# Performance work log

Hardware: AMD Instinct MI355X
Metric: run time of the kernel (lower is better)

## Reference

```python
import jax, jax.numpy as jnp
import numpy as np
import math

B, L, D, H = 2, 2048, 1024, 16
DH = D // H  # d_head = 64
FACTOR = 5


def setup_inputs() -> dict:
    key = jax.random.key(0)
    ks = jax.random.split(key, 6)
    s = 0.02
    x = jax.random.normal(ks[0], (B, L, D), jnp.float32)
    Wq = jax.random.normal(ks[1], (D, D), jnp.float32) * s
    bq = jnp.zeros((D,), jnp.float32)
    Wkv = jax.random.normal(ks[2], (2 * D, D), jnp.float32) * s
    bkv = jnp.zeros((2 * D,), jnp.float32)
    Wout = jax.random.normal(ks[3], (D, D), jnp.float32) * s
    bout = jnp.zeros((D,), jnp.float32)
    U = min(FACTOR * math.ceil(math.log(L)), L)  # 40
    index_sample = jax.random.randint(ks[4], (L, U), 0, L, dtype=jnp.int32)
    return {"x": x, "Wq": Wq, "bq": bq, "Wkv": Wkv, "bkv": bkv,
            "Wout": Wout, "bout": bout, "index_sample": index_sample,
            "factor": FACTOR}


def reference(x, Wq, bq, Wkv, bkv, Wout, bout, index_sample, factor):
    b, l, d = x.shape
    h, dh = H, DH
    scale = 1.0 / math.sqrt(dh)
    u = min(factor * math.ceil(math.log(l)), l)

    # projections (torch Linear: y = x @ W.T + b)
    Q = (x @ Wq.T + bq).reshape(b, l, h, dh).transpose(0, 2, 1, 3)   # [B,H,L,dh]
    KV = x @ Wkv.T + bkv
    K, V = jnp.split(KV, 2, axis=-1)
    K = K.reshape(b, l, h, dh).transpose(0, 2, 1, 3)                  # [B,H,L,dh]
    V = V.reshape(b, l, h, dh).transpose(0, 2, 1, 3)                  # [B,H,L,dh]

    # sampled QK: per query position l, dot with U sampled keys
    K_s = K[:, :, index_sample, :]                                    # [B,H,L,U,dh]
    QK = jnp.einsum('bhld,bhlud->bhlu', Q, K_s)                       # [B,H,L,U]
    M = QK.max(axis=-1) - QK.mean(axis=-1)                            # sparsity measure
    _, top_idx = jax.lax.top_k(M, u)                                  # [B,H,u]

    # full attention only for the top-u queries
    top_q = jnp.take_along_axis(Q, top_idx[..., None], axis=2)        # [B,H,u,dh]
    scores = jnp.einsum('bhud,bhkd->bhuk', top_q, K) * scale          # [B,H,u,L]
    attn = jax.nn.softmax(scores, axis=-1)
    ctx_update = jnp.einsum('bhuk,bhkd->bhud', attn, V)               # [B,H,u,dh]

    # mean-initialized context, scatter updates at top queries
    context = jnp.broadcast_to(V.mean(axis=2, keepdims=True), (b, h, l, dh))
    bI = jnp.arange(b)[:, None, None]
    hI = jnp.arange(h)[None, :, None]
    context = context.at[bI, hI, top_idx].set(ctx_update)             # [B,H,L,dh]

    context = context.transpose(0, 2, 1, 3).reshape(b, l, d)
    return context @ Wout.T + bout
```

## Files before the change

kernel.cpp:

```cpp
#include <hip/hip_runtime.h>
#include <math.h>

#define B_ 2
#define L_ 2048
#define D_ 1024
#define H_ 16
#define DH_ 64
#define U_ 40
#define SCALE_ 0.125f

typedef __attribute__((ext_vector_type(8))) short short8v;
typedef __attribute__((ext_vector_type(4))) float f32x4;
typedef __attribute__((ext_vector_type(4))) unsigned short ushort4v;

static __device__ __forceinline__ unsigned short bf16_rne(float f) {
  unsigned int u = __float_as_uint(f);
  u += 0x7fff + ((u >> 16) & 1);
  return (unsigned short)(u >> 16);
}
static __device__ __forceinline__ float bf16_f32(unsigned short h) {
  return __uint_as_float(((unsigned int)h) << 16);
}

static __device__ __forceinline__ void gload16(const unsigned short* src,
                                               unsigned short* lds) {
  __builtin_amdgcn_global_load_lds(
      (const __attribute__((address_space(1))) void*)src,
      (__attribute__((address_space(3))) void*)lds, 16, 0, 0);
}

#define FENCE asm volatile("" ::: "memory")
#define BARRIER                        \
  do {                                 \
    FENCE;                             \
    __builtin_amdgcn_s_barrier();      \
    FENCE;                             \
  } while (0)
#define LGKM0                                             \
  do {                                                    \
    asm volatile("s_waitcnt lgkmcnt(0)" ::: "memory");    \
    __builtin_amdgcn_sched_barrier(0);                    \
  } while (0)

__global__ __launch_bounds__(256) void split_all(
    const float* __restrict__ Wq, const float* __restrict__ Wkv,
    const float* __restrict__ X, unsigned short* __restrict__ Whi,
    unsigned short* __restrict__ Wlo, unsigned short* __restrict__ Xhi,
    unsigned short* __restrict__ Xlo, float* __restrict__ vmAcc, int nW) {
  if (blockIdx.x == 0) {
    for (int z = threadIdx.x; z < B_ * D_; z += 256) vmAcc[z] = 0.f;
  }
  int i = blockIdx.x * 256 + threadIdx.x;
  const int nq_q = (D_ * D_) / 4;
  float4 v;
  unsigned short *hi, *lo;
  int off;
  if (i < nW) {
    v = (i < nq_q) ? ((const float4*)Wq)[i] : ((const float4*)Wkv)[i - nq_q];
    hi = Whi; lo = Wlo; off = i;
  } else {
    off = i - nW;
    v = ((const float4*)X)[off];
    hi = Xhi; lo = Xlo;
  }
  float vv[4] = {v.x, v.y, v.z, v.w};
  ushort4v h, l;
#pragma unroll
  for (int e = 0; e < 4; ++e) {
    unsigned short hh = bf16_rne(vv[e]);
    h[e] = hh;
    l[e] = bf16_rne(vv[e] - bf16_f32(hh));
  }
  ((ushort4v*)hi)[off] = h;
  ((ushort4v*)lo)[off] = l;
}

__global__ __launch_bounds__(512, 2) void gemm_qkv_8ph(
    const unsigned short* __restrict__ Xhi,
    const unsigned short* __restrict__ Xlo,
    const unsigned short* __restrict__ Whi,
    const unsigned short* __restrict__ Wlo,
    const float* __restrict__ bq, const float* __restrict__ bkv,
    float* __restrict__ Qo, float* __restrict__ Ko, float* __restrict__ Vo,
    float* __restrict__ vmAcc) {
  __shared__ unsigned short LDS[3][20480];
  const int tid = threadIdx.x;
  const int lane = tid & 63;
  const int wave = tid >> 6;
  const int wm = wave >> 2, wn = wave & 3;
  const int row0 = blockIdx.y * 128;
  const int col0 = blockIdx.x * 192;

  f32x4 acc[4][3] = {};

  const unsigned short* gsrc[5];
#pragma unroll
  for (int r = 0; r < 5; ++r) {
    int c = wave + 8 * r;
    const unsigned short* base;
    int rowin, isA;
    if (c < 8)       { base = Xhi; rowin = c * 16;        isA = 1; }
    else if (c < 16) { base = Xlo; rowin = (c - 8) * 16;  isA = 1; }
    else if (c < 28) { base = Whi; rowin = (c - 16) * 16; isA = 0; }
    else             { base = Wlo; rowin = (c - 28) * 16; isA = 0; }
    rowin += (lane >> 2);
    int grow = (isA ? row0 : col0) + rowin;
    int seg = (lane & 3) ^ ((rowin >> 1) & 3);
    gsrc[r] = base + (size_t)grow * D_ + seg * 8;
  }

  const int fr_r = lane & 15;
  const int hs = lane >> 4;

#define RD_A(mi)                                                     \
  {                                                                  \
    int rr = wm * 64 + (mi) * 16 + fr_r;                             \
    int off = rr * 32 + ((hs ^ ((rr >> 1) & 3)) << 3);               \
    a_h[mi] = *(const short8v*)&Lc[off];                             \
    a_l[mi] = *(const short8v*)&Lc[4096 + off];                      \
  }
#define RD_B(ni)                                                     \
  {                                                                  \
    int rc = wn * 48 + (ni) * 16 + fr_r;                             \
    int off = rc * 32 + ((hs ^ ((rc >> 1) & 3)) << 3);               \
    b_h[ni] = *(const short8v*)&Lc[8192 + off];                      \
    b_l[ni] = *(const short8v*)&Lc[14336 + off];                     \
  }
#define MM3(mi, ni)                                                  \
  acc[mi][ni] = __builtin_amdgcn_mfma_f32_16x16x32_bf16(             \
      a_h[mi], b_h[ni], acc[mi][ni], 0, 0, 0);                       \
  acc[mi][ni] = __builtin_amdgcn_mfma_f32_16x16x32_bf16(             \
      a_h[mi], b_l[ni], acc[mi][ni], 0, 0, 0);                       \
  acc[mi][ni] = __builtin_amdgcn_mfma_f32_16x16x32_bf16(             \
      a_l[mi], b_h[ni], acc[mi][ni], 0, 0, 0);
#define STG(r, k0s, Ls) \
  gload16(gsrc[r] + (k0s), (Ls) + (wave + 8 * (r)) * 512)

  {
    unsigned short* L0 = &LDS[0][0];
    unsigned short* L1 = &LDS[1][0];
    STG(0, 0, L0); STG(1, 0, L0); STG(2, 0, L0); STG(3, 0, L0); STG(4, 0, L0);
    STG(0, 32, L1); STG(1, 32, L1); STG(2, 32, L1); STG(3, 32, L1);
    STG(4, 32, L1);
  }
  asm volatile("s_waitcnt vmcnt(5)" ::: "memory");
  BARRIER;

  for (int ks = 0; ks < 32; ++ks) {
    int cur = ks % 3;
    int stg = (ks + 2) % 3;
    int k0s = (ks + 2) * 32;
    unsigned short* Lc = &LDS[cur][0];
    unsigned short* Ls = &LDS[stg][0];
    short8v a_h[4], a_l[4], b_h[3], b_l[3];

    RD_A(0) RD_A(1) RD_B(0)
    if (ks < 30) { STG(0, k0s, Ls); STG(1, k0s, Ls); }
    BARRIER;
    LGKM0;
    __builtin_amdgcn_s_setprio(1);
    MM3(0, 0) MM3(1, 0)
    __builtin_amdgcn_s_setprio(0);
    BARRIER;

    RD_A(2) RD_B(1)
    if (ks < 30) { STG(2, k0s, Ls); STG(3, k0s, Ls); }
    BARRIER;
    LGKM0;
    __builtin_amdgcn_s_setprio(1);
    MM3(2, 0) MM3(0, 1) MM3(1, 1) MM3(2, 1)
    __builtin_amdgcn_s_setprio(0);
    BARRIER;

    RD_A(3) RD_B(2)
    if (ks < 30) { STG(4, k0s, Ls); }
    BARRIER;
    LGKM0;
    __builtin_amdgcn_s_setprio(1);
    MM3(3, 0) MM3(3, 1) MM3(0, 2) MM3(1, 2) MM3(2, 2) MM3(3, 2)
    __builtin_amdgcn_s_setprio(0);
    if (ks < 30) {
      asm volatile("s_waitcnt vmcnt(5)" ::: "memory");
    } else {
      asm volatile("s_waitcnt vmcnt(0)" ::: "memory");
    }
    BARRIER;
  }

#pragma unroll
  for (int ni = 0; ni < 3; ++ni) {
    int c = col0 + wn * 48 + ni * 16 + (lane & 15);
    int which = c >> 10;
    int jj = c & (D_ - 1);
    int h = jj >> 6, dh = jj & 63;
    float bias = (c < D_) ? bq[c] : bkv[c - D_];
    float* dst = (which == 0) ? Qo : ((which == 1) ? Ko : Vo);
#pragma unroll
    for (int mi = 0; mi < 4; ++mi) {
#pragma unroll
      for (int reg = 0; reg < 4; ++reg) {
        int r = row0 + wm * 64 + mi * 16 + ((lane >> 4) << 2) + reg;
        int b = r >> 11, l = r & (L_ - 1);
        dst[(((size_t)b * H_ + h) * L_ + l) * DH_ + dh] =
            acc[mi][ni][reg] + bias;
      }
    }
    if (which == 2) {
      float s = 0.f;
#pragma unroll
      for (int mi = 0; mi < 4; ++mi)
#pragma unroll
        for (int reg = 0; reg < 4; ++reg) s += acc[mi][ni][reg];
      s += __shfl_xor(s, 16);
      s += __shfl_xor(s, 32);
      if ((lane >> 4) == 0)
        atomicAdd(&vmAcc[(row0 >> 11) * D_ + jj], s + 64.0f * bias);
    }
  }
#undef RD_A
#undef RD_B
#undef MM3
#undef STG
}

__global__ __launch_bounds__(256) void gemm_qkv_fallback(
    const float* __restrict__ X,
    const unsigned short* __restrict__ Whi,
    const unsigned short* __restrict__ Wlo,
    const float* __restrict__ bq, const float* __restrict__ bkv,
    float* __restrict__ Qo, float* __restrict__ Ko, float* __restrict__ Vo,
    float* __restrict__ vmAcc) {
  __shared__ unsigned short Ah[128 * 32];
  __shared__ unsigned short Al[128 * 32];
  __shared__ unsigned short Bh[128 * 32];
  __shared__ unsigned short Bl[128 * 32];
  const int tid = threadIdx.x;
  const int lane = tid & 63;
  const int wave = tid >> 6;
  const int wm = wave >> 1, wn = wave & 1;
  const int row0 = blockIdx.y * 128;
  const int col0 = blockIdx.x * 128;

  f32x4 acc[4][4] = {};

  const int grow = lane >> 2;
  const int gg = lane & 3;

  for (int k0 = 0; k0 < D_; k0 += 32) {
#pragma unroll
    for (int j = 0; j < 2; ++j) {
      int c = wave + 4 * j;
      int row = c * 16 + grow;
      int gsrc = (gg ^ ((row >> 1) & 3)) << 3;
      size_t soffB = (size_t)(col0 + row) * D_ + k0 + gsrc;
      gload16(Whi + soffB, Bh + c * 512);
      gload16(Wlo + soffB, Bl + c * 512);
    }
#pragma unroll
    for (int rep = 0; rep < 2; ++rep) {
      int task = tid + rep * 256;
      int row = task >> 2;
      int gt = task & 3;
      const float* s = X + (size_t)(row0 + row) * D_ + k0 + gt * 8;
      float4 a0 = *(const float4*)s;
      float4 a1 = *(const float4*)(s + 4);
      float av[8] = {a0.x, a0.y, a0.z, a0.w, a1.x, a1.y, a1.z, a1.w};
      short8v hseg, lseg;
#pragma unroll
      for (int e = 0; e < 8; ++e) {
        unsigned short hh = bf16_rne(av[e]);
        hseg[e] = (short)hh;
        lseg[e] = (short)bf16_rne(av[e] - bf16_f32(hh));
      }
      int dst = row * 32 + ((gt ^ ((row >> 1) & 3)) << 3);
      *(short8v*)&Ah[dst] = hseg;
      *(short8v*)&Al[dst] = lseg;
    }
    __syncthreads();

    short8v a_h[4], a_l[4], b_h[4], b_l[4];
    const int hs = lane >> 4;
#pragma unroll
    for (int mi = 0; mi < 4; ++mi) {
      int rr = wm * 64 + mi * 16 + (lane & 15);
      int off = rr * 32 + ((hs ^ ((rr >> 1) & 3)) << 3);
      a_h[mi] = *(const short8v*)&Ah[off];
      a_l[mi] = *(const short8v*)&Al[off];
    }
#pragma unroll
    for (int ni = 0; ni < 4; ++ni) {
      int rc = wn * 64 + ni * 16 + (lane & 15);
      int off = rc * 32 + ((hs ^ ((rc >> 1) & 3)) << 3);
      b_h[ni] = *(const short8v*)&Bh[off];
      b_l[ni] = *(const short8v*)&Bl[off];
    }
#pragma unroll
    for (int mi = 0; mi < 4; ++mi)
#pragma unroll
      for (int ni = 0; ni < 4; ++ni) {
        acc[mi][ni] = __builtin_amdgcn_mfma_f32_16x16x32_bf16(
            a_h[mi], b_h[ni], acc[mi][ni], 0, 0, 0);
        acc[mi][ni] = __builtin_amdgcn_mfma_f32_16x16x32_bf16(
            a_h[mi], b_l[ni], acc[mi][ni], 0, 0, 0);
        acc[mi][ni] = __builtin_amdgcn_mfma_f32_16x16x32_bf16(
            a_l[mi], b_h[ni], acc[mi][ni], 0, 0, 0);
      }
    __syncthreads();
  }

#pragma unroll
  for (int ni = 0; ni < 4; ++ni) {
    int c = col0 + wn * 64 + ni * 16 + (lane & 15);
    int which = c >> 10;
    int jj = c & (D_ - 1);
    int h = jj >> 6, dh = jj & 63;
    float bias = (c < D_) ? bq[c] : bkv[c - D_];
    float* dst = (which == 0) ? Qo : ((which == 1) ? Ko : Vo);
#pragma unroll
    for (int mi = 0; mi < 4; ++mi) {
#pragma unroll
      for (int reg = 0; reg < 4; ++reg) {
        int r = row0 + wm * 64 + mi * 16 + ((lane >> 4) << 2) + reg;
        int b = r >> 11, l = r & (L_ - 1);
        dst[(((size_t)b * H_ + h) * L_ + l) * DH_ + dh] =
            acc[mi][ni][reg] + bias;
      }
    }
    if (which == 2) {
      float s = 0.f;
#pragma unroll
      for (int mi = 0; mi < 4; ++mi)
#pragma unroll
        for (int reg = 0; reg < 4; ++reg) s += acc[mi][ni][reg];
      s += __shfl_xor(s, 16);
      s += __shfl_xor(s, 32);
      if ((lane >> 4) == 0)
        atomicAdd(&vmAcc[(row0 >> 11) * D_ + jj], s + 64.0f * bias);
    }
  }
}

__global__ __launch_bounds__(256) void base_kernel(
    const float* __restrict__ vmAcc, const float* __restrict__ Wout,
    const float* __restrict__ bout, float* __restrict__ baseOut,
    float* __restrict__ vmeanM) {
  int bid = blockIdx.x;
  int b = bid >> 4, jc = bid & 15;
  int t = threadIdx.x;
  int j = jc * 64 + (t & 63);
  int isl = t >> 6;
  __shared__ float vm[D_];
  __shared__ float red[256];
  for (int i = t; i < D_; i += 256) vm[i] = vmAcc[b * D_ + i] * (1.0f / L_);
  __syncthreads();
  if (jc == 0)
    for (int i = t; i < D_; i += 256) vmeanM[b * D_ + i] = vm[i];
  float s = 0.f;
  const float* wr = Wout + (size_t)j * D_ + isl * 256;
  const float* vv = vm + isl * 256;
  for (int i = 0; i < 256; i += 4) {
    float4 w = *(const float4*)(wr + i);
    s += vv[i] * w.x + vv[i + 1] * w.y + vv[i + 2] * w.z + vv[i + 3] * w.w;
  }
  red[t] = s; __syncthreads();
  if (isl == 0)
    baseOut[b * D_ + j] =
        red[t] + red[t + 64] + red[t + 128] + red[t + 192] + bout[j];
}

__global__ __launch_bounds__(256) void bcast_out(
    const float* __restrict__ baseIn, float* __restrict__ out) {
  size_t i4 = (size_t)blockIdx.x * 256 + threadIdx.x;
  size_t i = i4 * 4;
  int b = (int)(i >> 21);
  int col = (int)(i & (D_ - 1));
  *(float4*)(out + i) = *(const float4*)(baseIn + b * D_ + col);
}

__global__ __launch_bounds__(256) void sample_m(
    const float* __restrict__ Q, const float* __restrict__ Kt,
    const int* __restrict__ idx, float* __restrict__ Mv) {
  int t = threadIdx.x;
  int w = t >> 6, lane = t & 63;
  int subl = lane >> 4, d16 = lane & 15;
  int gl = blockIdx.x * 16 + w * 4 + subl;
  int bh = gl >> 11, l = gl & (L_ - 1);
  const float4* Kb4 = (const float4*)(Kt + (size_t)bh * L_ * DH_);
  float4 q4 = ((const float4*)(Q + (size_t)gl * DH_))[d16];
  const int* irow = idx + l * U_;
  float mx = -INFINITY, sm = 0.f;
#pragma unroll 8
  for (int u = 0; u < U_; ++u) {
    int kl = irow[u];
    float4 k4 = Kb4[kl * 16 + d16];
    float p = q4.x * k4.x + q4.y * k4.y + q4.z * k4.z + q4.w * k4.w;
    p += __shfl_xor(p, 1);
    p += __shfl_xor(p, 2);
    p += __shfl_xor(p, 4);
    p += __shfl_xor(p, 8);
    mx = fmaxf(mx, p);
    sm += p;
  }
  if (d16 == 0) Mv[gl] = mx - sm * (1.0f / U_);
}

__global__ __launch_bounds__(64) void topk_kernel(
    const float* __restrict__ Mv, int* __restrict__ topIdx) {
  __shared__ float vals[L_];
  int lane = threadIdx.x;
  int bh = blockIdx.x;
  for (int j = 0; j < 32; ++j)
    vals[j * 64 + lane] = Mv[(size_t)bh * L_ + j * 64 + lane];
  __syncthreads();
  for (int it = 0; it < U_; ++it) {
    float bv = -INFINITY;
    int bi = 0x7fffffff;
    for (int j = 0; j < 32; ++j) {
      int i = j * 64 + lane;
      float v = vals[i];
      if (v > bv) { bv = v; bi = i; }
    }
#pragma unroll
    for (int off = 32; off > 0; off >>= 1) {
      float ov = __shfl_xor(bv, off);
      int oi = __shfl_xor(bi, off);
      if (ov > bv || (ov == bv && oi < bi)) { bv = ov; bi = oi; }
    }
    if (lane == 0) topIdx[bh * U_ + it] = bi;
    vals[bi] = -INFINITY;
    __syncthreads();
  }
}

__global__ __launch_bounds__(256) void attn_corr(
    const float* __restrict__ Q, const float* __restrict__ Kt,
    const float* __restrict__ Vt, const int* __restrict__ topIdx,
    const float* __restrict__ vmeanM, const float* __restrict__ Wout,
    float* __restrict__ out) {
  int qc = blockIdx.x;
  int bh = blockIdx.y;
  int b = bh >> 4, h = bh & (H_ - 1);
  __shared__ float Qs[5][DH_];
  __shared__ float Sv[5][L_];
  __shared__ float part[4][5][DH_];
  __shared__ float inv[5];
  __shared__ float dv[5][DH_];
  __shared__ int lq[5];
  int t = threadIdx.x;
  int lane = t & 63, w = t >> 6;

  if (t < 80) {
    int q = t >> 4, c4 = t & 15;
    int ql = topIdx[bh * U_ + qc * 5 + q];
    *(float4*)&Qs[q][c4 * 4] =
        *(const float4*)&Q[((size_t)bh * L_ + ql) * DH_ + c4 * 4];
  }
  if (t < 5) lq[t] = topIdx[bh * U_ + qc * 5 + t];
  __syncthreads();

  const float* Kb = Kt + (size_t)bh * L_ * DH_;
  for (int kc = 0; kc < 8; ++kc) {
    int key = kc * 256 + t;
    const float* kr = Kb + (size_t)key * DH_;
    float acc[5];
#pragma unroll
    for (int q = 0; q < 5; ++q) acc[q] = 0.f;
#pragma unroll
    for (int i4 = 0; i4 < 16; ++i4) {
      float4 k4 = *(const float4*)(kr + i4 * 4);
#pragma unroll
      for (int q = 0; q < 5; ++q) {
        float4 qv = *(const float4*)&Qs[q][i4 * 4];
        acc[q] += k4.x * qv.x + k4.y * qv.y + k4.z * qv.z + k4.w * qv.w;
      }
    }
#pragma unroll
    for (int q = 0; q < 5; ++q) Sv[q][key] = acc[q] * SCALE_;
  }
  __syncthreads();

#pragma unroll
  for (int rep = 0; rep < 2; ++rep) {
    int r = (rep == 0) ? w : (w == 0 ? 4 : -1);
    if (r >= 0) {
      float mx = -INFINITY;
      for (int j = 0; j < 32; ++j) mx = fmaxf(mx, Sv[r][j * 64 + lane]);
#pragma unroll
      for (int off = 1; off < 64; off <<= 1)
        mx = fmaxf(mx, __shfl_xor(mx, off));
      float sm = 0.f;
      for (int j = 0; j < 32; ++j) {
        float e = __expf(Sv[r][j * 64 + lane] - mx);
        Sv[r][j * 64 + lane] = e;
        sm += e;
      }
#pragma unroll
      for (int off = 1; off < 64; off <<= 1) sm += __shfl_xor(sm, off);
      if (lane == 0) inv[r] = 1.0f / sm;
    }
  }
  __syncthreads();

  {
    const float* vb = Vt + ((size_t)bh * L_ + w * 512) * DH_ + lane;
    float acc[5];
#pragma unroll
    for (int q = 0; q < 5; ++q) acc[q] = 0.f;
    for (int k4 = 0; k4 < 128; ++k4) {
      float v0 = vb[(k4 * 4 + 0) * DH_];
      float v1 = vb[(k4 * 4 + 1) * DH_];
      float v2 = vb[(k4 * 4 + 2) * DH_];
      float v3 = vb[(k4 * 4 + 3) * DH_];
      int k = w * 512 + k4 * 4;
#pragma unroll
      for (int q = 0; q < 5; ++q) {
        float4 p4 = *(const float4*)&Sv[q][k];
        acc[q] += p4.x * v0 + p4.y * v1 + p4.z * v2 + p4.w * v3;
      }
    }
#pragma unroll
    for (int q = 0; q < 5; ++q) part[w][q][lane] = acc[q];
  }
  __syncthreads();

  for (int o = t; o < 5 * DH_; o += 256) {
    int q = o >> 6, dh = o & 63;
    float s = (part[0][q][dh] + part[1][q][dh]) +
              (part[2][q][dh] + part[3][q][dh]);
    dv[q][dh] = s * inv[q] - vmeanM[b * D_ + h * DH_ + dh];
  }
  __syncthreads();

  int sub = t & 3;
  int jbase = t >> 2;
#pragma unroll
  for (int jc = 0; jc < 16; ++jc) {
    int j = jc * 64 + jbase;
    const float* wr = Wout + (size_t)j * D_ + h * DH_ + sub * 16;
    float4 w0 = ((const float4*)wr)[0];
    float4 w1 = ((const float4*)wr)[1];
    float4 w2 = ((const float4*)wr)[2];
    float4 w3 = ((const float4*)wr)[3];
#pragma unroll
    for (int q = 0; q < 5; ++q) {
      const float* dq = &dv[q][sub * 16];
      float s = dq[0] * w0.x + dq[1] * w0.y + dq[2] * w0.z + dq[3] * w0.w +
                dq[4] * w1.x + dq[5] * w1.y + dq[6] * w1.z + dq[7] * w1.w +
                dq[8] * w2.x + dq[9] * w2.y + dq[10] * w2.z + dq[11] * w2.w +
                dq[12] * w3.x + dq[13] * w3.y + dq[14] * w3.z + dq[15] * w3.w;
      s += __shfl_xor(s, 1);
      s += __shfl_xor(s, 2);
      if (sub == 0)
        atomicAdd(out + ((size_t)b * L_ + lq[q]) * D_ + j, s);
    }
  }
}

extern "C" void kernel_launch(void* const* d_in, const int* in_sizes, int n_in,
                              void* d_out, int out_size, void* d_ws,
                              size_t ws_size, hipStream_t stream) {
  const float* x    = (const float*)d_in[0];
  const float* Wq   = (const float*)d_in[1];
  const float* bq   = (const float*)d_in[2];
  const float* Wkv  = (const float*)d_in[3];
  const float* bkv  = (const float*)d_in[4];
  const float* Wout = (const float*)d_in[5];
  const float* bout = (const float*)d_in[6];
  const int*   idx  = (const int*)d_in[7];
  float* out = (float*)d_out;

  float* ws = (float*)d_ws;
  const size_t NQ = (size_t)B_ * H_ * L_ * DH_;
  float* Q  = ws;
  float* Kt = Q + NQ;
  float* Vt = Kt + NQ;
  unsigned short* Whi = (unsigned short*)(Vt + NQ);
  unsigned short* Wlo = Whi + (size_t)3 * D_ * D_;
  unsigned short* Xhi = Wlo + (size_t)3 * D_ * D_;
  unsigned short* Xlo = Xhi + NQ;
  float* Mv     = Vt + NQ;
  float* vmeanM = Mv + (size_t)B_ * H_ * L_;
  float* baseB  = vmeanM + B_ * D_;
  int*   topIdx = (int*)(baseB + B_ * D_);
  float* vmAcc = out;

  const bool xsplit = ws_size >= ((size_t)76 << 20);
  const int nW = 3 * D_ * D_ / 4;
  const int nX = (int)(NQ / 4);

  if (xsplit) {
    split_all<<<dim3((nW + nX) / 256), dim3(256), 0, stream>>>(
        Wq, Wkv, x, Whi, Wlo, Xhi, Xlo, vmAcc, nW);
    gemm_qkv_8ph<<<dim3(3 * D_ / 192, B_ * L_ / 128), dim3(512), 0, stream>>>(
        Xhi, Xlo, Whi, Wlo, bq, bkv, Q, Kt, Vt, vmAcc);
  } else {
    split_all<<<dim3(nW / 256), dim3(256), 0, stream>>>(Wq, Wkv, x, Whi, Wlo,
                                                        Xhi, Xlo, vmAcc, nW);
    gemm_qkv_fallback<<<dim3(3 * D_ / 128, B_ * L_ / 128), dim3(256), 0,
                        stream>>>(x, Whi, Wlo, bq, bkv, Q, Kt, Vt, vmAcc);
  }
  base_kernel<<<dim3(B_ * 16), dim3(256), 0, stream>>>(vmAcc, Wout, bout,
                                                       baseB, vmeanM);
  bcast_out<<<dim3(B_ * L_ * D_ / 1024), dim3(256), 0, stream>>>(baseB, out);
  sample_m<<<dim3(B_ * H_ * L_ / 16), dim3(256), 0, stream>>>(Q, Kt, idx, Mv);
  topk_kernel<<<dim3(B_ * H_), dim3(64), 0, stream>>>(Mv, topIdx);
  attn_corr<<<dim3(8, 32), dim3(256), 0, stream>>>(Q, Kt, Vt, topIdx, vmeanM,
                                                   Wout, out);
}
```

Before: 245.5 us.

## Simplify QKV GEMM pipeline and merge independent small kernels into shared launches

The QKV GEMM main loop drops the three-phase interleaving of LDS reads, staging loads, barriers and setprio. Each iteration now issues all async global-to-LDS stages up front, reads every A/B fragment, then runs the full MFMA block with one barrier, and launch bounds become (512,1). Separately, the sample-M kernel is merged with the mean-context base kernel, and the output broadcast is merged with top-k, each pair using a block-index split. This cuts two launches and lets independent work overlap. The risk is that the coarser GEMM schedule hides LDS latency worse than the hand-interleaved version.

```diff
diff --git a/kernel.cpp b/kernel.cpp
--- a/kernel.cpp
+++ b/kernel.cpp
@@ -29,17 +29,16 @@
       (__attribute__((address_space(3))) void*)lds, 16, 0, 0);
 }
 
-#define FENCE asm volatile("" ::: "memory")
-#define BARRIER                        \
-  do {                                 \
-    FENCE;                             \
-    __builtin_amdgcn_s_barrier();      \
-    FENCE;                             \
+#define BARRIER                                  \
+  do {                                           \
+    asm volatile("" ::: "memory");               \
+    __builtin_amdgcn_s_barrier();                \
+    asm volatile("" ::: "memory");               \
   } while (0)
-#define LGKM0                                             \
-  do {                                                    \
-    asm volatile("s_waitcnt lgkmcnt(0)" ::: "memory");    \
-    __builtin_amdgcn_sched_barrier(0);                    \
+#define LGKM0                                          \
+  do {                                                 \
+    asm volatile("s_waitcnt lgkmcnt(0)" ::: "memory"); \
+    __builtin_amdgcn_sched_barrier(0);                 \
   } while (0)
 
 __global__ __launch_bounds__(256) void split_all(
@@ -75,7 +74,7 @@
   ((ushort4v*)lo)[off] = l;
 }
 
-__global__ __launch_bounds__(512, 2) void gemm_qkv_8ph(
+__global__ __launch_bounds__(512, 1) void gemm_qkv_pipe(
     const unsigned short* __restrict__ Xhi,
     const unsigned short* __restrict__ Xlo,
     const unsigned short* __restrict__ Whi,
@@ -112,27 +111,6 @@
   const int fr_r = lane & 15;
   const int hs = lane >> 4;
 
-#define RD_A(mi)                                                     \
-  {                                                                  \
-    int rr = wm * 64 + (mi) * 16 + fr_r;                             \
-    int off = rr * 32 + ((hs ^ ((rr >> 1) & 3)) << 3);               \
-    a_h[mi] = *(const short8v*)&Lc[off];                             \
-    a_l[mi] = *(const short8v*)&Lc[4096 + off];                      \
-  }
-#define RD_B(ni)                                                     \
-  {                                                                  \
-    int rc = wn * 48 + (ni) * 16 + fr_r;                             \
-    int off = rc * 32 + ((hs ^ ((rc >> 1) & 3)) << 3);               \
-    b_h[ni] = *(const short8v*)&Lc[8192 + off];                      \
-    b_l[ni] = *(const short8v*)&Lc[14336 + off];                     \
-  }
-#define MM3(mi, ni)                                                  \
-  acc[mi][ni] = __builtin_amdgcn_mfma_f32_16x16x32_bf16(             \
-      a_h[mi], b_h[ni], acc[mi][ni], 0, 0, 0);                       \
-  acc[mi][ni] = __builtin_amdgcn_mfma_f32_16x16x32_bf16(             \
-      a_h[mi], b_l[ni], acc[mi][ni], 0, 0, 0);                       \
-  acc[mi][ni] = __builtin_amdgcn_mfma_f32_16x16x32_bf16(             \
-      a_l[mi], b_h[ni], acc[mi][ni], 0, 0, 0);
 #define STG(r, k0s, Ls) \
   gload16(gsrc[r] + (k0s), (Ls) + (wave + 8 * (r)) * 512)
 
@@ -147,38 +125,44 @@
   BARRIER;
 
   for (int ks = 0; ks < 32; ++ks) {
-    int cur = ks % 3;
-    int stg = (ks + 2) % 3;
+    unsigned short* Lc = &LDS[ks % 3][0];
+    unsigned short* Ls = &LDS[(ks + 2) % 3][0];
     int k0s = (ks + 2) * 32;
-    unsigned short* Lc = &LDS[cur][0];
-    unsigned short* Ls = &LDS[stg][0];
+
+    if (ks < 30) {
+      STG(0, k0s, Ls); STG(1, k0s, Ls); STG(2, k0s, Ls); STG(3, k0s, Ls);
+      STG(4, k0s, Ls);
+    }
+
     short8v a_h[4], a_l[4], b_h[3], b_l[3];
-
-    RD_A(0) RD_A(1) RD_B(0)
-    if (ks < 30) { STG(0, k0s, Ls); STG(1, k0s, Ls); }
-    BARRIER;
+#pragma unroll
+    for (int mi = 0; mi < 4; ++mi) {
+      int rr = wm * 64 + mi * 16 + fr_r;
+      int off = rr * 32 + ((hs ^ ((rr >> 1) & 3)) << 3);
+      a_h[mi] = *(const short8v*)&Lc[off];
+      a_l[mi] = *(const short8v*)&Lc[4096 + off];
+    }
+#pragma unroll
+    for (int ni = 0; ni < 3; ++ni) {
+      int rc = wn * 48 + ni * 16 + fr_r;
+      int off = rc * 32 + ((hs ^ ((rc >> 1) & 3)) << 3);
+      b_h[ni] = *(const short8v*)&Lc[8192 + off];
+      b_l[ni] = *(const short8v*)&Lc[14336 + off];
+    }
+
+#pragma unroll
+    for (int mi = 0; mi < 4; ++mi)
+#pragma unroll
+      for (int ni = 0; ni < 3; ++ni) {
+        acc[mi][ni] = __builtin_amdgcn_mfma_f32_16x16x32_bf16(
+            a_h[mi], b_h[ni], acc[mi][ni], 0, 0, 0);
+        acc[mi][ni] = __builtin_amdgcn_mfma_f32_16x16x32_bf16(
+            a_h[mi], b_l[ni], acc[mi][ni], 0, 0, 0);
+        acc[mi][ni] = __builtin_amdgcn_mfma_f32_16x16x32_bf16(
+            a_l[mi], b_h[ni], acc[mi][ni], 0, 0, 0);
+      }
+
     LGKM0;
-    __builtin_amdgcn_s_setprio(1);
-    MM3(0, 0) MM3(1, 0)
-    __builtin_amdgcn_s_setprio(0);
-    BARRIER;
-
-    RD_A(2) RD_B(1)
-    if (ks < 30) { STG(2, k0s, Ls); STG(3, k0s, Ls); }
-    BARRIER;
-    LGKM0;
-    __builtin_amdgcn_s_setprio(1);
-    MM3(2, 0) MM3(0, 1) MM3(1, 1) MM3(2, 1)
-    __builtin_amdgcn_s_setprio(0);
-    BARRIER;
-
-    RD_A(3) RD_B(2)
-    if (ks < 30) { STG(4, k0s, Ls); }
-    BARRIER;
-    LGKM0;
-    __builtin_amdgcn_s_setprio(1);
-    MM3(3, 0) MM3(3, 1) MM3(0, 2) MM3(1, 2) MM3(2, 2) MM3(3, 2)
-    __builtin_amdgcn_s_setprio(0);
     if (ks < 30) {
       asm volatile("s_waitcnt vmcnt(5)" ::: "memory");
     } else {
@@ -217,9 +201,6 @@
         atomicAdd(&vmAcc[(row0 >> 11) * D_ + jj], s + 64.0f * bias);
     }
   }
-#undef RD_A
-#undef RD_B
-#undef MM3
 #undef STG
 }
 
@@ -340,95 +321,95 @@
   }
 }
 
-__global__ __launch_bounds__(256) void base_kernel(
+__global__ __launch_bounds__(256) void sample_base(
+    const float* __restrict__ Q, const float* __restrict__ Kt,
+    const int* __restrict__ idx, float* __restrict__ Mv,
     const float* __restrict__ vmAcc, const float* __restrict__ Wout,
     const float* __restrict__ bout, float* __restrict__ baseOut,
     float* __restrict__ vmeanM) {
-  int bid = blockIdx.x;
-  int b = bid >> 4, jc = bid & 15;
   int t = threadIdx.x;
-  int j = jc * 64 + (t & 63);
-  int isl = t >> 6;
-  __shared__ float vm[D_];
-  __shared__ float red[256];
-  for (int i = t; i < D_; i += 256) vm[i] = vmAcc[b * D_ + i] * (1.0f / L_);
-  __syncthreads();
-  if (jc == 0)
-    for (int i = t; i < D_; i += 256) vmeanM[b * D_ + i] = vm[i];
-  float s = 0.f;
-  const float* wr = Wout + (size_t)j * D_ + isl * 256;
-  const float* vv = vm + isl * 256;
-  for (int i = 0; i < 256; i += 4) {
-    float4 w = *(const float4*)(wr + i);
-    s += vv[i] * w.x + vv[i + 1] * w.y + vv[i + 2] * w.z + vv[i + 3] * w.w;
-  }
-  red[t] = s; __syncthreads();
-  if (isl == 0)
-    baseOut[b * D_ + j] =
-        red[t] + red[t + 64] + red[t + 128] + red[t + 192] + bout[j];
-}
-
-__global__ __launch_bounds__(256) void bcast_out(
-    const float* __restrict__ baseIn, float* __restrict__ out) {
-  size_t i4 = (size_t)blockIdx.x * 256 + threadIdx.x;
-  size_t i = i4 * 4;
-  int b = (int)(i >> 21);
-  int col = (int)(i & (D_ - 1));
-  *(float4*)(out + i) = *(const float4*)(baseIn + b * D_ + col);
-}
-
-__global__ __launch_bounds__(256) void sample_m(
-    const float* __restrict__ Q, const float* __restrict__ Kt,
-    const int* __restrict__ idx, float* __restrict__ Mv) {
+  if (blockIdx.x < 4096) {
+    int w = t >> 6, lane = t & 63;
+    int subl = lane >> 4, d16 = lane & 15;
+    int gl = blockIdx.x * 16 + w * 4 + subl;
+    int bh = gl >> 11, l = gl & (L_ - 1);
+    const float4* Kb4 = (const float4*)(Kt + (size_t)bh * L_ * DH_);
+    float4 q4 = ((const float4*)(Q + (size_t)gl * DH_))[d16];
+    const int* irow = idx + l * U_;
+    float mx = -INFINITY, sm = 0.f;
+#pragma unroll 8
+    for (int u = 0; u < U_; ++u) {
+      int kl = irow[u];
+      float4 k4 = Kb4[kl * 16 + d16];
+      float p = q4.x * k4.x + q4.y * k4.y + q4.z * k4.z + q4.w * k4.w;
+      p += __shfl_xor(p, 1);
+      p += __shfl_xor(p, 2);
+      p += __shfl_xor(p, 4);
+      p += __shfl_xor(p, 8);
+      mx = fmaxf(mx, p);
+      sm += p;
+    }
+    if (d16 == 0) Mv[gl] = mx - sm * (1.0f / U_);
+  } else {
+    int bid = blockIdx.x - 4096;
+    int b = bid >> 4, jc = bid & 15;
+    int j = jc * 64 + (t & 63);
+    int isl = t >> 6;
+    __shared__ float vm[D_];
+    __shared__ float red[256];
+    for (int i = t; i < D_; i += 256) vm[i] = vmAcc[b * D_ + i] * (1.0f / L_);
+    __syncthreads();
+    if (jc == 0)
+      for (int i = t; i < D_; i += 256) vmeanM[b * D_ + i] = vm[i];
+    float s = 0.f;
+    const float* wr = Wout + (size_t)j * D_ + isl * 256;
+    const float* vv = vm + isl * 256;
+    for (int i = 0; i < 256; i += 4) {
+      float4 w = *(const float4*)(wr + i);
+      s += vv[i] * w.x + vv[i + 1] * w.y + vv[i + 2] * w.z + vv[i + 3] * w.w;
+    }
+    red[t] = s;
+    __syncthreads();
+    if (isl == 0)
+      baseOut[b * D_ + j] =
+          red[t] + red[t + 64] + red[t + 128] + red[t + 192] + bout[j];
+  }
+}
+
+__global__ __launch_bounds__(256) void bcast_topk(
+    const float* __restrict__ baseIn, float* __restrict__ out,
+    const float* __restrict__ Mv, int* __restrict__ topIdx) {
   int t = threadIdx.x;
-  int w = t >> 6, lane = t & 63;
-  int subl = lane >> 4, d16 = lane & 15;
-  int gl = blockIdx.x * 16 + w * 4 + subl;
-  int bh = gl >> 11, l = gl & (L_ - 1);
-  const float4* Kb4 = (const float4*)(Kt + (size_t)bh * L_ * DH_);
-  float4 q4 = ((const float4*)(Q + (size_t)gl * DH_))[d16];
-  const int* irow = idx + l * U_;
-  float mx = -INFINITY, sm = 0.f;
-#pragma unroll 8
-  for (int u = 0; u < U_; ++u) {
-    int kl = irow[u];
-    float4 k4 = Kb4[kl * 16 + d16];
-    float p = q4.x * k4.x + q4.y * k4.y + q4.z * k4.z + q4.w * k4.w;
-    p += __shfl_xor(p, 1);
-    p += __shfl_xor(p, 2);
-    p += __shfl_xor(p, 4);
-    p += __shfl_xor(p, 8);
-    mx = fmaxf(mx, p);
-    sm += p;
-  }
-  if (d16 == 0) Mv[gl] = mx - sm * (1.0f / U_);
-}
-
-__global__ __launch_bounds__(64) void topk_kernel(
-    const float* __restrict__ Mv, int* __restrict__ topIdx) {
-  __shared__ float vals[L_];
-  int lane = threadIdx.x;
-  int bh = blockIdx.x;
-  for (int j = 0; j < 32; ++j)
-    vals[j * 64 + lane] = Mv[(size_t)bh * L_ + j * 64 + lane];
-  __syncthreads();
-  for (int it = 0; it < U_; ++it) {
-    float bv = -INFINITY;
-    int bi = 0x7fffffff;
-    for (int j = 0; j < 32; ++j) {
-      int i = j * 64 + lane;
-      float v = vals[i];
-      if (v > bv) { bv = v; bi = i; }
-    }
-#pragma unroll
-    for (int off = 32; off > 0; off >>= 1) {
-      float ov = __shfl_xor(bv, off);
-      int oi = __shfl_xor(bi, off);
-      if (ov > bv || (ov == bv && oi < bi)) { bv = ov; bi = oi; }
-    }
-    if (lane == 0) topIdx[bh * U_ + it] = bi;
-    vals[bi] = -INFINITY;
+  if (blockIdx.x < 4096) {
+    size_t i4 = (size_t)blockIdx.x * 256 + t;
+    size_t i = i4 * 4;
+    int b = (int)(i >> 21);
+    int col = (int)(i & (D_ - 1));
+    *(float4*)(out + i) = *(const float4*)(baseIn + b * D_ + col);
+  } else {
+    __shared__ float vals[L_];
+    int lane = t & 63;
+    int bh = blockIdx.x - 4096;
+    for (int j = t; j < L_; j += 256) vals[j] = Mv[(size_t)bh * L_ + j];
     __syncthreads();
+    for (int it = 0; it < U_; ++it) {
+      float bv = -INFINITY;
+      int bi = 0x7fffffff;
+      for (int j = 0; j < 32; ++j) {
+        int i = j * 64 + lane;
+        float v = vals[i];
+        if (v > bv) { bv = v; bi = i; }
+      }
+#pragma unroll
+      for (int off = 32; off > 0; off >>= 1) {
+        float ov = __shfl_xor(bv, off);
+        int oi = __shfl_xor(bi, off);
+        if (ov > bv || (ov == bv && oi < bi)) { bv = ov; bi = oi; }
+      }
+      if (t == 0) topIdx[bh * U_ + it] = bi;
+      vals[bi] = -INFINITY;
+      __syncthreads();
+    }
   }
 }
 
@@ -591,19 +572,18 @@
   if (xsplit) {
     split_all<<<dim3((nW + nX) / 256), dim3(256), 0, stream>>>(
         Wq, Wkv, x, Whi, Wlo, Xhi, Xlo, vmAcc, nW);
-    gemm_qkv_8ph<<<dim3(3 * D_ / 192, B_ * L_ / 128), dim3(512), 0, stream>>>(
-        Xhi, Xlo, Whi, Wlo, bq, bkv, Q, Kt, Vt, vmAcc);
+    gemm_qkv_pipe<<<dim3(3 * D_ / 192, B_ * L_ / 128), dim3(512), 0,
+                    stream>>>(Xhi, Xlo, Whi, Wlo, bq, bkv, Q, Kt, Vt, vmAcc);
   } else {
     split_all<<<dim3(nW / 256), dim3(256), 0, stream>>>(Wq, Wkv, x, Whi, Wlo,
                                                         Xhi, Xlo, vmAcc, nW);
     gemm_qkv_fallback<<<dim3(3 * D_ / 128, B_ * L_ / 128), dim3(256), 0,
                         stream>>>(x, Whi, Wlo, bq, bkv, Q, Kt, Vt, vmAcc);
   }
-  base_kernel<<<dim3(B_ * 16), dim3(256), 0, stream>>>(vmAcc, Wout, bout,
-                                                       baseB, vmeanM);
-  bcast_out<<<dim3(B_ * L_ * D_ / 1024), dim3(256), 0, stream>>>(baseB, out);
-  sample_m<<<dim3(B_ * H_ * L_ / 16), dim3(256), 0, stream>>>(Q, Kt, idx, Mv);
-  topk_kernel<<<dim3(B_ * H_), dim3(64), 0, stream>>>(Mv, topIdx);
+  sample_base<<<dim3(4096 + B_ * 16), dim3(256), 0, stream>>>(
+      Q, Kt, idx, Mv, vmAcc, Wout, bout, baseB, vmeanM);
+  bcast_topk<<<dim3(4096 + B_ * H_), dim3(256), 0, stream>>>(baseB, out, Mv,
+                                                             topIdx);
   attn_corr<<<dim3(8, 32), dim3(256), 0, stream>>>(Q, Kt, Vt, topIdx, vmeanM,
                                                    Wout, out);
 }
```

Result: faster. 238.6 us (-2.8%).
